# Kernel optimization log

Hardware: AMD Instinct MI355X
Metric: run time of the kernel (lower is better)

Reference implementation:

```python
import jax, jax.numpy as jnp
import numpy as np
import math

B, S, D = 8, 2048, 1024  # batch, seq_len, d_model (num_heads=1 -> d_k=d_v=D)

def _trunc_normal(key, shape, fan_in, fan_out):
    std = math.sqrt(2.0 / (fan_in + fan_out))
    return jax.random.truncated_normal(key, -3.0, 3.0, shape, jnp.float32) * std

def setup_inputs() -> dict:
    key = jax.random.key(0)
    kx, kq, kk, kv, ko = jax.random.split(key, 5)
    return {
        "in_features": jax.random.normal(kx, (B, S, D), jnp.float32),
        "Wq": _trunc_normal(kq, (D, D), D, D),  # Linear stores (out, in)
        "Wk": _trunc_normal(kk, (D, D), D, D),
        "Wv": _trunc_normal(kv, (D, D), D, D),
        "Wo": _trunc_normal(ko, (D, D), D, D),
    }

def reference(in_features, Wq, Wk, Wv, Wo):
    d_k = Wq.shape[0]
    scale = 1.0 / math.sqrt(d_k)
    x = in_features  # [B,S,D]; num_heads=1 so head split/merge are identities
    Q = x @ Wq.T  # [B,S,d_k]
    K = x @ Wk.T
    V = x @ Wv.T
    scores = jnp.einsum('bqd,bkd->bqk', Q, K) * scale  # [B,S,S]
    seq_len = x.shape[-2]
    causal = jnp.tril(jnp.ones((seq_len, seq_len), dtype=bool))
    scores = jnp.where(causal, scores, -jnp.inf)
    attn = jax.nn.softmax(scores, axis=-1)  # stable max-shift softmax, same as run_softmax
    out = jnp.einsum('bqk,bkd->bqd', attn, V)  # [B,S,d_v]
    return out @ Wo.T  # [B,S,D]
```

## Files before the change

kernel.cpp:

```cpp
#include <hip/hip_runtime.h>
#include <hip/hip_bf16.h>
#include <cstdint>


typedef short    bf16x8 __attribute__((ext_vector_type(8)));
typedef _Float16 f16x8  __attribute__((ext_vector_type(8)));
typedef _Float16 f16x4  __attribute__((ext_vector_type(4)));
typedef float    f32x4  __attribute__((ext_vector_type(4)));

#define S_LEN 2048
#define D_DIM 1024
#define M_ROWS 16384
#define NT_Q 16
#define SLOTS 136
#define SLOT_ELEMS 16384
#define PBATCH ((size_t)SLOTS * SLOT_ELEMS)

__device__ __forceinline__ ushort f32_to_bf16_rne(float f) {
    uint32_t u = __float_as_uint(f);
    uint32_t r = (u + 0x7FFFu + ((u >> 16) & 1u)) >> 16;
    return (ushort)r;
}

__device__ __forceinline__ void gload_lds16(const void* g, void* l) {
    __builtin_amdgcn_global_load_lds(
        (const __attribute__((address_space(1))) uint32_t*)(const uint32_t*)g,
        (__attribute__((address_space(3))) uint32_t*)(uint32_t*)l, 16, 0, 0);
}

__global__ void cast_f32_bf16(const float* __restrict__ in,
                              ushort* __restrict__ out, int n4) {
    int i = blockIdx.x * blockDim.x + threadIdx.x;
    if (i < n4) {
        float4 v = ((const float4*)in)[i];
        ushort4 o;
        o.x = f32_to_bf16_rne(v.x);
        o.y = f32_to_bf16_rne(v.y);
        o.z = f32_to_bf16_rne(v.z);
        o.w = f32_to_bf16_rne(v.w);
        ((ushort4*)out)[i] = o;
    }
}

template <int MODE>
__global__ __launch_bounds__(256)
void gemm_bt(const ushort* __restrict__ A, const ushort* __restrict__ B,
             void* __restrict__ C) {
    __shared__ ushort As[128 * 32];
    __shared__ ushort Bs[128 * 32];

    const int t  = threadIdx.x;
    const int tm = blockIdx.x;
    const int tn = blockIdx.y;
    const int l  = t & 63;
    const int w  = t >> 6;
    const int wr = w >> 1, wc = w & 1;
    const int lr = l & 15;
    const int lk = (l >> 4) << 3;

    f32x4 acc[4][4] = {};

    const int arow = t >> 2;
    const int akc  = (t & 3) << 3;
    const ushort* Ag = A + (size_t)(tm * 128 + arow) * D_DIM + akc;
    const ushort* Bg = B + (size_t)(tn * 128 + arow) * D_DIM + akc;
    ushort* Al = &As[arow * 32 + akc];
    ushort* Bl = &Bs[arow * 32 + akc];

    for (int k0 = 0; k0 < D_DIM; k0 += 32) {
        __syncthreads();
        gload_lds16(Ag + k0,              Al);
        gload_lds16(Ag + k0 + 64 * D_DIM, Al + 64 * 32);
        gload_lds16(Bg + k0,              Bl);
        gload_lds16(Bg + k0 + 64 * D_DIM, Bl + 64 * 32);
        __syncthreads();

        bf16x8 af[4], bf[4];
#pragma unroll
        for (int m = 0; m < 4; ++m)
            af[m] = *(const bf16x8*)&As[(wr * 64 + m * 16 + lr) * 32 + lk];
#pragma unroll
        for (int n = 0; n < 4; ++n)
            bf[n] = *(const bf16x8*)&Bs[(wc * 64 + n * 16 + lr) * 32 + lk];
#pragma unroll
        for (int n = 0; n < 4; ++n)
#pragma unroll
            for (int m = 0; m < 4; ++m)
                acc[n][m] = __builtin_amdgcn_mfma_f32_16x16x32_bf16(
                    bf[n], af[m], acc[n][m], 0, 0, 0);
    }

    const int cr = (l >> 4) << 2;
#pragma unroll
    for (int n = 0; n < 4; ++n) {
#pragma unroll
        for (int m = 0; m < 4; ++m) {
            const int row  = tm * 128 + wr * 64 + m * 16 + lr;
            const int col0 = tn * 128 + wc * 64 + n * 16 + cr;
            f32x4 v = acc[n][m];
            if (MODE == 0) {
                ushort4 o;
                o.x = f32_to_bf16_rne(v[0]);
                o.y = f32_to_bf16_rne(v[1]);
                o.z = f32_to_bf16_rne(v[2]);
                o.w = f32_to_bf16_rne(v[3]);
                *(ushort4*)((ushort*)C + (size_t)row * D_DIM + col0) = o;
            } else if (MODE == 2) {
                *(f32x4*)((float*)C + (size_t)row * D_DIM + col0) = v;
            } else {
                const int b = row >> 11;
                const int s = row & 2047;
                _Float16* Vt = (_Float16*)C;
                size_t base = ((size_t)b * D_DIM + col0) * S_LEN + s;
#pragma unroll
                for (int r = 0; r < 4; ++r)
                    Vt[base + (size_t)r * S_LEN] = (_Float16)v[r];
            }
        }
    }
}

__global__ __launch_bounds__(256)
void gemm_qk(const ushort* __restrict__ Q, const ushort* __restrict__ K,
             _Float16* __restrict__ P) {
    __shared__ ushort As[128 * 32];
    __shared__ ushort Bs[128 * 32];

    const int b = blockIdx.y;
    const int s = blockIdx.x;
    int tm = (int)((sqrtf(8.0f * (float)s + 1.0f) - 1.0f) * 0.5f);
    while ((tm + 1) * (tm + 2) / 2 <= s) ++tm;
    while (tm * (tm + 1) / 2 > s) --tm;
    const int tn = s - tm * (tm + 1) / 2;

    const int t  = threadIdx.x;
    const int l  = t & 63;
    const int w  = t >> 6;
    const int wr = w >> 1, wc = w & 1;
    const int lr = l & 15;
    const int lk = (l >> 4) << 3;

    f32x4 acc[4][4] = {};

    const int arow = t >> 2;
    const int akc  = (t & 3) << 3;
    const ushort* Ag = Q + ((size_t)b * S_LEN + tm * 128 + arow) * D_DIM + akc;
    const ushort* Bg = K + ((size_t)b * S_LEN + tn * 128 + arow) * D_DIM + akc;
    ushort* Al = &As[arow * 32 + akc];
    ushort* Bl = &Bs[arow * 32 + akc];

    for (int k0 = 0; k0 < D_DIM; k0 += 32) {
        __syncthreads();
        gload_lds16(Ag + k0,              Al);
        gload_lds16(Ag + k0 + 64 * D_DIM, Al + 64 * 32);
        gload_lds16(Bg + k0,              Bl);
        gload_lds16(Bg + k0 + 64 * D_DIM, Bl + 64 * 32);
        __syncthreads();

        bf16x8 af[4], bf[4];
#pragma unroll
        for (int m = 0; m < 4; ++m)
            af[m] = *(const bf16x8*)&As[(wr * 64 + m * 16 + lr) * 32 + lk];
#pragma unroll
        for (int n = 0; n < 4; ++n)
            bf[n] = *(const bf16x8*)&Bs[(wc * 64 + n * 16 + lr) * 32 + lk];
#pragma unroll
        for (int n = 0; n < 4; ++n)
#pragma unroll
            for (int m = 0; m < 4; ++m)
                acc[n][m] = __builtin_amdgcn_mfma_f32_16x16x32_bf16(
                    bf[n], af[m], acc[n][m], 0, 0, 0);
    }

    _Float16* slot = P + (size_t)b * PBATCH + (size_t)s * SLOT_ELEMS;
    const int cr = (l >> 4) << 2;
    const float scale = 0.03125f;
#pragma unroll
    for (int n = 0; n < 4; ++n) {
#pragma unroll
        for (int m = 0; m < 4; ++m) {
            const int row_l  = wr * 64 + m * 16 + lr;
            const int col0_l = wc * 64 + n * 16 + cr;
            f32x4 v = acc[n][m];
            f16x4 o;
#pragma unroll
            for (int r = 0; r < 4; ++r) {
                float sv = v[r] * scale;
                if (tm == tn && (col0_l + r) > row_l) sv = -30000.0f;
                o[r] = (_Float16)sv;
            }
            *(f16x4*)(slot + (size_t)row_l * 128 + col0_l) = o;
        }
    }
}

__global__ __launch_bounds__(256)
void softmax_rows(_Float16* __restrict__ P) {
    const int b  = blockIdx.y;
    const int q  = blockIdx.x;
    const int tm = q >> 7;
    const int nchunk = (tm + 1) * 16;
    _Float16* row = P + (size_t)b * PBATCH +
                    ((size_t)(tm * (tm + 1) / 2)) * SLOT_ELEMS +
                    (size_t)(q & 127) * 128;

    const int t = threadIdx.x;
    const bool active = t < nchunk;
    _Float16* addr = row + (size_t)(t >> 4) * SLOT_ELEMS + (t & 15) * 8;

    float v[8];
    float mx = -1e30f;
    if (active) {
        f16x8 h = *(const f16x8*)addr;
#pragma unroll
        for (int i = 0; i < 8; ++i) {
            v[i] = (float)h[i];
            mx = fmaxf(mx, v[i]);
        }
    }
#pragma unroll
    for (int d = 1; d < 64; d <<= 1) mx = fmaxf(mx, __shfl_xor(mx, d));
    __shared__ float redm[4], reds[4];
    if ((t & 63) == 0) redm[t >> 6] = mx;
    __syncthreads();
    mx = fmaxf(fmaxf(redm[0], redm[1]), fmaxf(redm[2], redm[3]));

    float sum = 0.0f;
    if (active) {
#pragma unroll
        for (int i = 0; i < 8; ++i) {
            v[i] = __expf(v[i] - mx);
            sum += v[i];
        }
    }
#pragma unroll
    for (int d = 1; d < 64; d <<= 1) sum += __shfl_xor(sum, d);
    if ((t & 63) == 0) reds[t >> 6] = sum;
    __syncthreads();
    sum = reds[0] + reds[1] + reds[2] + reds[3];
    const float inv = 1.0f / sum;

    if (active) {
        f16x8 h;
#pragma unroll
        for (int i = 0; i < 8; ++i) h[i] = (_Float16)(v[i] * inv);
        *(f16x8*)addr = h;
    }
}

__global__ __launch_bounds__(256)
void gemm_pv(const _Float16* __restrict__ P, const _Float16* __restrict__ Vt,
             ushort* __restrict__ O) {
    __shared__ _Float16 As[128 * 32];
    __shared__ _Float16 Bs[128 * 32];

    const int b  = blockIdx.y;
    const int tm = NT_Q - 1 - (blockIdx.x >> 3);
    const int dn = blockIdx.x & 7;
    const int KN = (tm + 1) * 128;

    const int t  = threadIdx.x;
    const int l  = t & 63;
    const int w  = t >> 6;
    const int wr = w >> 1, wc = w & 1;
    const int lr = l & 15;
    const int lk = (l >> 4) << 3;

    f32x4 acc[4][4] = {};

    const int arow = t >> 2;
    const int akc  = (t & 3) << 3;
    const _Float16* Prow = P + (size_t)b * PBATCH +
                           ((size_t)(tm * (tm + 1) / 2)) * SLOT_ELEMS;
    const _Float16* Vb = Vt + ((size_t)b * D_DIM + dn * 128 + arow) * S_LEN;
    _Float16* Al = &As[arow * 32 + akc];
    _Float16* Bl = &Bs[arow * 32 + akc];

    for (int k0 = 0; k0 < KN; k0 += 32) {
        const _Float16* Ag = Prow + (size_t)(k0 >> 7) * SLOT_ELEMS +
                             (size_t)arow * 128 + (k0 & 127) + akc;
        __syncthreads();
        gload_lds16(Ag,            Al);
        gload_lds16(Ag + 64 * 128, Al + 64 * 32);
        gload_lds16(Vb + k0 + akc,               Bl);
        gload_lds16(Vb + k0 + akc + 64 * S_LEN,  Bl + 64 * 32);
        __syncthreads();

        f16x8 af[4], bf[4];
#pragma unroll
        for (int m = 0; m < 4; ++m)
            af[m] = *(const f16x8*)&As[(wr * 64 + m * 16 + lr) * 32 + lk];
#pragma unroll
        for (int n = 0; n < 4; ++n)
            bf[n] = *(const f16x8*)&Bs[(wc * 64 + n * 16 + lr) * 32 + lk];
#pragma unroll
        for (int n = 0; n < 4; ++n)
#pragma unroll
            for (int m = 0; m < 4; ++m)
                acc[n][m] = __builtin_amdgcn_mfma_f32_16x16x32_f16(
                    bf[n], af[m], acc[n][m], 0, 0, 0);
    }

    const int cr = (l >> 4) << 2;
#pragma unroll
    for (int n = 0; n < 4; ++n) {
#pragma unroll
        for (int m = 0; m < 4; ++m) {
            const int row  = tm * 128 + wr * 64 + m * 16 + lr;
            const int col0 = dn * 128 + wc * 64 + n * 16 + cr;
            f32x4 v = acc[n][m];
            ushort4 o;
            o.x = f32_to_bf16_rne(v[0]);
            o.y = f32_to_bf16_rne(v[1]);
            o.z = f32_to_bf16_rne(v[2]);
            o.w = f32_to_bf16_rne(v[3]);
            *(ushort4*)(O + ((size_t)b * S_LEN + row) * D_DIM + col0) = o;
        }
    }
}

extern "C" void kernel_launch(void* const* d_in, const int* in_sizes, int n_in,
                              void* d_out, int out_size, void* d_ws,
                              size_t ws_size, hipStream_t stream) {
    const float* x  = (const float*)d_in[0];
    const float* Wq = (const float*)d_in[1];
    const float* Wk = (const float*)d_in[2];
    const float* Wv = (const float*)d_in[3];
    const float* Wo = (const float*)d_in[4];

    char* ws = (char*)d_ws;
    size_t off = 0;
    ushort*    xb  = (ushort*)(ws + off);    off += (size_t)M_ROWS * D_DIM * 2;
    ushort*    Wqb = (ushort*)(ws + off);    off += (size_t)D_DIM * D_DIM * 2;
    ushort*    Wkb = (ushort*)(ws + off);    off += (size_t)D_DIM * D_DIM * 2;
    ushort*    Wvb = (ushort*)(ws + off);    off += (size_t)D_DIM * D_DIM * 2;
    ushort*    Wob = (ushort*)(ws + off);    off += (size_t)D_DIM * D_DIM * 2;
    ushort*    Qb  = (ushort*)(ws + off);    off += (size_t)M_ROWS * D_DIM * 2;
    ushort*    Kb  = (ushort*)(ws + off);    off += (size_t)M_ROWS * D_DIM * 2;
    _Float16*  Vtb = (_Float16*)(ws + off);  off += (size_t)M_ROWS * D_DIM * 2;
    _Float16*  Pb  = (_Float16*)(ws + off);  off += (size_t)8 * PBATCH * 2;

    cast_f32_bf16<<<(M_ROWS * D_DIM / 4 + 255) / 256, 256, 0, stream>>>(
        x, xb, M_ROWS * D_DIM / 4);
    cast_f32_bf16<<<(D_DIM * D_DIM / 4 + 255) / 256, 256, 0, stream>>>(
        Wq, Wqb, D_DIM * D_DIM / 4);
    cast_f32_bf16<<<(D_DIM * D_DIM / 4 + 255) / 256, 256, 0, stream>>>(
        Wk, Wkb, D_DIM * D_DIM / 4);
    cast_f32_bf16<<<(D_DIM * D_DIM / 4 + 255) / 256, 256, 0, stream>>>(
        Wv, Wvb, D_DIM * D_DIM / 4);
    cast_f32_bf16<<<(D_DIM * D_DIM / 4 + 255) / 256, 256, 0, stream>>>(
        Wo, Wob, D_DIM * D_DIM / 4);

    dim3 gg(M_ROWS / 128, D_DIM / 128);
    gemm_bt<0><<<gg, 256, 0, stream>>>(xb, Wqb, Qb);
    gemm_bt<0><<<gg, 256, 0, stream>>>(xb, Wkb, Kb);
    gemm_bt<1><<<gg, 256, 0, stream>>>(xb, Wvb, Vtb);

    gemm_qk<<<dim3(SLOTS, 8), 256, 0, stream>>>(Qb, Kb, Pb);
    softmax_rows<<<dim3(S_LEN, 8), 256, 0, stream>>>(Pb);
    gemm_pv<<<dim3(128, 8), 256, 0, stream>>>(Pb, Vtb, xb);

    gemm_bt<2><<<gg, 256, 0, stream>>>(xb, Wob, (float*)d_out);
}
```

Measured before the change: 532.1 us.

## Fuse QKV projections, widen PV tiles, swizzle block order, batch weight casts

The three QKV projection GEMMs become one 512-thread kernel that loads each x tile once and multiplies it against all three weight tiles, cutting x reads by a factor of three. The PV GEMM now computes a 128x256 output tile per block, halving P reloads at the cost of more accumulator registers. Block indices in the projection, QK and output GEMMs are remapped so neighbouring blocks land on different XCDs for better cache locality. The four weight casts are merged into one launch. The larger register footprint in the fused kernels may lower occupancy.

```diff
diff --git a/kernel.cpp b/kernel.cpp
--- a/kernel.cpp
+++ b/kernel.cpp
@@ -42,75 +42,117 @@
     }
 }
 
-template <int MODE>
-__global__ __launch_bounds__(256)
-void gemm_bt(const ushort* __restrict__ A, const ushort* __restrict__ B,
-             void* __restrict__ C) {
+__global__ void cast4_f32_bf16(const float* __restrict__ w0,
+                               const float* __restrict__ w1,
+                               const float* __restrict__ w2,
+                               const float* __restrict__ w3,
+                               ushort* __restrict__ o0, ushort* __restrict__ o1,
+                               ushort* __restrict__ o2, ushort* __restrict__ o3,
+                               int n4) {
+    const int s = blockIdx.y;
+    const float* in  = (s == 0) ? w0 : (s == 1) ? w1 : (s == 2) ? w2 : w3;
+    ushort*      out = (s == 0) ? o0 : (s == 1) ? o1 : (s == 2) ? o2 : o3;
+    int i = blockIdx.x * blockDim.x + threadIdx.x;
+    if (i < n4) {
+        float4 v = ((const float4*)in)[i];
+        ushort4 o;
+        o.x = f32_to_bf16_rne(v.x);
+        o.y = f32_to_bf16_rne(v.y);
+        o.z = f32_to_bf16_rne(v.z);
+        o.w = f32_to_bf16_rne(v.w);
+        ((ushort4*)out)[i] = o;
+    }
+}
+
+__global__ __launch_bounds__(512)
+void gemm_qkv3(const ushort* __restrict__ A, const ushort* __restrict__ Wq,
+               const ushort* __restrict__ Wk, const ushort* __restrict__ Wv,
+               ushort* __restrict__ Qo, ushort* __restrict__ Ko,
+               _Float16* __restrict__ Vt) {
     __shared__ ushort As[128 * 32];
-    __shared__ ushort Bs[128 * 32];
+    __shared__ ushort Bs[3][128 * 32];
+
+    const int bid = blockIdx.x;
+    const int g   = (bid & 7) * 128 + (bid >> 3);
+    const int tm  = g >> 3;
+    const int tn  = g & 7;
 
     const int t  = threadIdx.x;
-    const int tm = blockIdx.x;
-    const int tn = blockIdx.y;
     const int l  = t & 63;
     const int w  = t >> 6;
-    const int wr = w >> 1, wc = w & 1;
+    const int wr = w >> 2;
+    const int wc = w & 3;
     const int lr = l & 15;
     const int lk = (l >> 4) << 3;
 
-    f32x4 acc[4][4] = {};
+    f32x4 acc[3][4][2] = {};
 
     const int arow = t >> 2;
-    const int akc  = (t & 3) << 3;
-    const ushort* Ag = A + (size_t)(tm * 128 + arow) * D_DIM + akc;
-    const ushort* Bg = B + (size_t)(tn * 128 + arow) * D_DIM + akc;
-    ushort* Al = &As[arow * 32 + akc];
-    ushort* Bl = &Bs[arow * 32 + akc];
+    const int acol = (t & 3) << 3;
+    const ushort* Ag  = A  + (size_t)(tm * 128 + arow) * D_DIM + acol;
+    const ushort* Bg0 = Wq + (size_t)(tn * 128 + arow) * D_DIM + acol;
+    const ushort* Bg1 = Wk + (size_t)(tn * 128 + arow) * D_DIM + acol;
+    const ushort* Bg2 = Wv + (size_t)(tn * 128 + arow) * D_DIM + acol;
+    ushort* Al  = &As[t * 8];
+    ushort* Bl0 = &Bs[0][t * 8];
+    ushort* Bl1 = &Bs[1][t * 8];
+    ushort* Bl2 = &Bs[2][t * 8];
 
     for (int k0 = 0; k0 < D_DIM; k0 += 32) {
         __syncthreads();
-        gload_lds16(Ag + k0,              Al);
-        gload_lds16(Ag + k0 + 64 * D_DIM, Al + 64 * 32);
-        gload_lds16(Bg + k0,              Bl);
-        gload_lds16(Bg + k0 + 64 * D_DIM, Bl + 64 * 32);
-        __syncthreads();
-
-        bf16x8 af[4], bf[4];
+        gload_lds16(Ag + k0,  Al);
+        gload_lds16(Bg0 + k0, Bl0);
+        gload_lds16(Bg1 + k0, Bl1);
+        gload_lds16(Bg2 + k0, Bl2);
+        __syncthreads();
+
+        bf16x8 af[4];
 #pragma unroll
         for (int m = 0; m < 4; ++m)
             af[m] = *(const bf16x8*)&As[(wr * 64 + m * 16 + lr) * 32 + lk];
 #pragma unroll
-        for (int n = 0; n < 4; ++n)
-            bf[n] = *(const bf16x8*)&Bs[(wc * 64 + n * 16 + lr) * 32 + lk];
-#pragma unroll
-        for (int n = 0; n < 4; ++n)
-#pragma unroll
-            for (int m = 0; m < 4; ++m)
-                acc[n][m] = __builtin_amdgcn_mfma_f32_16x16x32_bf16(
-                    bf[n], af[m], acc[n][m], 0, 0, 0);
+        for (int w3 = 0; w3 < 3; ++w3) {
+            bf16x8 b0 = *(const bf16x8*)&Bs[w3][(wc * 32 + lr) * 32 + lk];
+            bf16x8 b1 = *(const bf16x8*)&Bs[w3][(wc * 32 + 16 + lr) * 32 + lk];
+#pragma unroll
+            for (int m = 0; m < 4; ++m) {
+                acc[w3][m][0] = __builtin_amdgcn_mfma_f32_16x16x32_bf16(
+                    b0, af[m], acc[w3][m][0], 0, 0, 0);
+                acc[w3][m][1] = __builtin_amdgcn_mfma_f32_16x16x32_bf16(
+                    b1, af[m], acc[w3][m][1], 0, 0, 0);
+            }
+        }
     }
 
     const int cr = (l >> 4) << 2;
 #pragma unroll
-    for (int n = 0; n < 4; ++n) {
-#pragma unroll
-        for (int m = 0; m < 4; ++m) {
+    for (int m = 0; m < 4; ++m) {
+#pragma unroll
+        for (int n = 0; n < 2; ++n) {
             const int row  = tm * 128 + wr * 64 + m * 16 + lr;
-            const int col0 = tn * 128 + wc * 64 + n * 16 + cr;
-            f32x4 v = acc[n][m];
-            if (MODE == 0) {
+            const int col0 = tn * 128 + wc * 32 + n * 16 + cr;
+            {
+                f32x4 v = acc[0][m][n];
                 ushort4 o;
                 o.x = f32_to_bf16_rne(v[0]);
                 o.y = f32_to_bf16_rne(v[1]);
                 o.z = f32_to_bf16_rne(v[2]);
                 o.w = f32_to_bf16_rne(v[3]);
-                *(ushort4*)((ushort*)C + (size_t)row * D_DIM + col0) = o;
-            } else if (MODE == 2) {
-                *(f32x4*)((float*)C + (size_t)row * D_DIM + col0) = v;
-            } else {
+                *(ushort4*)(Qo + (size_t)row * D_DIM + col0) = o;
+            }
+            {
+                f32x4 v = acc[1][m][n];
+                ushort4 o;
+                o.x = f32_to_bf16_rne(v[0]);
+                o.y = f32_to_bf16_rne(v[1]);
+                o.z = f32_to_bf16_rne(v[2]);
+                o.w = f32_to_bf16_rne(v[3]);
+                *(ushort4*)(Ko + (size_t)row * D_DIM + col0) = o;
+            }
+            {
+                f32x4 v = acc[2][m][n];
                 const int b = row >> 11;
                 const int s = row & 2047;
-                _Float16* Vt = (_Float16*)C;
                 size_t base = ((size_t)b * D_DIM + col0) * S_LEN + s;
 #pragma unroll
                 for (int r = 0; r < 4; ++r)
@@ -127,7 +169,8 @@
     __shared__ ushort Bs[128 * 32];
 
     const int b = blockIdx.y;
-    const int s = blockIdx.x;
+    const int x = blockIdx.x;
+    const int s = (x & 7) * 17 + (x >> 3);
     int tm = (int)((sqrtf(8.0f * (float)s + 1.0f) - 1.0f) * 0.5f);
     while ((tm + 1) * (tm + 2) / 2 <= s) ++tm;
     while (tm * (tm + 1) / 2 > s) --tm;
@@ -249,15 +292,17 @@
 }
 
 __global__ __launch_bounds__(256)
-void gemm_pv(const _Float16* __restrict__ P, const _Float16* __restrict__ Vt,
-             ushort* __restrict__ O) {
+void gemm_pv2(const _Float16* __restrict__ P, const _Float16* __restrict__ Vt,
+              ushort* __restrict__ O) {
     __shared__ _Float16 As[128 * 32];
-    __shared__ _Float16 Bs[128 * 32];
-
-    const int b  = blockIdx.y;
-    const int tm = NT_Q - 1 - (blockIdx.x >> 3);
-    const int dn = blockIdx.x & 7;
-    const int KN = (tm + 1) * 128;
+    __shared__ _Float16 Bs[256 * 32];
+
+    const int b   = blockIdx.y;
+    const int x   = blockIdx.x;
+    const int g   = (x & 7) * 8 + (x >> 3);
+    const int tm  = NT_Q - 1 - (g >> 2);
+    const int dn2 = g & 3;
+    const int KN  = (tm + 1) * 128;
 
     const int t  = threadIdx.x;
     const int l  = t & 63;
@@ -266,49 +311,50 @@
     const int lr = l & 15;
     const int lk = (l >> 4) << 3;
 
-    f32x4 acc[4][4] = {};
+    f32x4 acc[4][8] = {};
 
     const int arow = t >> 2;
-    const int akc  = (t & 3) << 3;
+    const int acol = (t & 3) << 3;
     const _Float16* Prow = P + (size_t)b * PBATCH +
                            ((size_t)(tm * (tm + 1) / 2)) * SLOT_ELEMS;
-    const _Float16* Vb = Vt + ((size_t)b * D_DIM + dn * 128 + arow) * S_LEN;
-    _Float16* Al = &As[arow * 32 + akc];
-    _Float16* Bl = &Bs[arow * 32 + akc];
+    const _Float16* Vb = Vt + ((size_t)b * D_DIM + dn2 * 256 + arow) * S_LEN;
+    _Float16* Al = &As[t * 8];
+    _Float16* Bl = &Bs[t * 8];
 
     for (int k0 = 0; k0 < KN; k0 += 32) {
         const _Float16* Ag = Prow + (size_t)(k0 >> 7) * SLOT_ELEMS +
-                             (size_t)arow * 128 + (k0 & 127) + akc;
+                             (size_t)arow * 128 + (k0 & 127) + acol;
         __syncthreads();
         gload_lds16(Ag,            Al);
         gload_lds16(Ag + 64 * 128, Al + 64 * 32);
-        gload_lds16(Vb + k0 + akc,               Bl);
-        gload_lds16(Vb + k0 + akc + 64 * S_LEN,  Bl + 64 * 32);
-        __syncthreads();
-
-        f16x8 af[4], bf[4];
+        gload_lds16(Vb + k0 + acol,                 Bl);
+        gload_lds16(Vb + k0 + acol + 64 * S_LEN,    Bl + 64 * 32);
+        gload_lds16(Vb + k0 + acol + 128 * S_LEN,   Bl + 128 * 32);
+        gload_lds16(Vb + k0 + acol + 192 * S_LEN,   Bl + 192 * 32);
+        __syncthreads();
+
+        f16x8 af[4];
 #pragma unroll
         for (int m = 0; m < 4; ++m)
             af[m] = *(const f16x8*)&As[(wr * 64 + m * 16 + lr) * 32 + lk];
 #pragma unroll
-        for (int n = 0; n < 4; ++n)
-            bf[n] = *(const f16x8*)&Bs[(wc * 64 + n * 16 + lr) * 32 + lk];
-#pragma unroll
-        for (int n = 0; n < 4; ++n)
+        for (int n = 0; n < 8; ++n) {
+            f16x8 bv = *(const f16x8*)&Bs[(wc * 128 + n * 16 + lr) * 32 + lk];
 #pragma unroll
             for (int m = 0; m < 4; ++m)
-                acc[n][m] = __builtin_amdgcn_mfma_f32_16x16x32_f16(
-                    bf[n], af[m], acc[n][m], 0, 0, 0);
+                acc[m][n] = __builtin_amdgcn_mfma_f32_16x16x32_f16(
+                    bv, af[m], acc[m][n], 0, 0, 0);
+        }
     }
 
     const int cr = (l >> 4) << 2;
 #pragma unroll
-    for (int n = 0; n < 4; ++n) {
-#pragma unroll
-        for (int m = 0; m < 4; ++m) {
+    for (int m = 0; m < 4; ++m) {
+#pragma unroll
+        for (int n = 0; n < 8; ++n) {
             const int row  = tm * 128 + wr * 64 + m * 16 + lr;
-            const int col0 = dn * 128 + wc * 64 + n * 16 + cr;
-            f32x4 v = acc[n][m];
+            const int col0 = dn2 * 256 + wc * 128 + n * 16 + cr;
+            f32x4 v = acc[m][n];
             ushort4 o;
             o.x = f32_to_bf16_rne(v[0]);
             o.y = f32_to_bf16_rne(v[1]);
@@ -317,6 +363,67 @@
             *(ushort4*)(O + ((size_t)b * S_LEN + row) * D_DIM + col0) = o;
         }
     }
+}
+
+__global__ __launch_bounds__(256)
+void gemm_out(const ushort* __restrict__ A, const ushort* __restrict__ B,
+              float* __restrict__ C) {
+    __shared__ ushort As[128 * 32];
+    __shared__ ushort Bs[128 * 32];
+
+    const int bid = blockIdx.x;
+    const int g   = (bid & 7) * 128 + (bid >> 3);
+    const int tm  = g >> 3;
+    const int tn  = g & 7;
+
+    const int t  = threadIdx.x;
+    const int l  = t & 63;
+    const int w  = t >> 6;
+    const int wr = w >> 1, wc = w & 1;
+    const int lr = l & 15;
+    const int lk = (l >> 4) << 3;
+
+    f32x4 acc[4][4] = {};
+
+    const int arow = t >> 2;
+    const int akc  = (t & 3) << 3;
+    const ushort* Ag = A + (size_t)(tm * 128 + arow) * D_DIM + akc;
+    const ushort* Bg = B + (size_t)(tn * 128 + arow) * D_DIM + akc;
+    ushort* Al = &As[arow * 32 + akc];
+    ushort* Bl = &Bs[arow * 32 + akc];
+
+    for (int k0 = 0; k0 < D_DIM; k0 += 32) {
+        __syncthreads();
+        gload_lds16(Ag + k0,              Al);
+        gload_lds16(Ag + k0 + 64 * D_DIM, Al + 64 * 32);
+        gload_lds16(Bg + k0,              Bl);
+        gload_lds16(Bg + k0 + 64 * D_DIM, Bl + 64 * 32);
+        __syncthreads();
+
+        bf16x8 af[4], bf[4];
+#pragma unroll
+        for (int m = 0; m < 4; ++m)
+            af[m] = *(const bf16x8*)&As[(wr * 64 + m * 16 + lr) * 32 + lk];
+#pragma unroll
+        for (int n = 0; n < 4; ++n)
+            bf[n] = *(const bf16x8*)&Bs[(wc * 64 + n * 16 + lr) * 32 + lk];
+#pragma unroll
+        for (int n = 0; n < 4; ++n)
+#pragma unroll
+            for (int m = 0; m < 4; ++m)
+                acc[n][m] = __builtin_amdgcn_mfma_f32_16x16x32_bf16(
+                    bf[n], af[m], acc[n][m], 0, 0, 0);
+    }
+
+    const int cr = (l >> 4) << 2;
+#pragma unroll
+    for (int n = 0; n < 4; ++n)
+#pragma unroll
+        for (int m = 0; m < 4; ++m) {
+            const int row  = tm * 128 + wr * 64 + m * 16 + lr;
+            const int col0 = tn * 128 + wc * 64 + n * 16 + cr;
+            *(f32x4*)(C + (size_t)row * D_DIM + col0) = acc[n][m];
+        }
 }
 
 extern "C" void kernel_launch(void* const* d_in, const int* in_sizes, int n_in,
@@ -342,23 +449,14 @@
 
     cast_f32_bf16<<<(M_ROWS * D_DIM / 4 + 255) / 256, 256, 0, stream>>>(
         x, xb, M_ROWS * D_DIM / 4);
-    cast_f32_bf16<<<(D_DIM * D_DIM / 4 + 255) / 256, 256, 0, stream>>>(
-        Wq, Wqb, D_DIM * D_DIM / 4);
-    cast_f32_bf16<<<(D_DIM * D_DIM / 4 + 255) / 256, 256, 0, stream>>>(
-        Wk, Wkb, D_DIM * D_DIM / 4);
-    cast_f32_bf16<<<(D_DIM * D_DIM / 4 + 255) / 256, 256, 0, stream>>>(
-        Wv, Wvb, D_DIM * D_DIM / 4);
-    cast_f32_bf16<<<(D_DIM * D_DIM / 4 + 255) / 256, 256, 0, stream>>>(
-        Wo, Wob, D_DIM * D_DIM / 4);
-
-    dim3 gg(M_ROWS / 128, D_DIM / 128);
-    gemm_bt<0><<<gg, 256, 0, stream>>>(xb, Wqb, Qb);
-    gemm_bt<0><<<gg, 256, 0, stream>>>(xb, Wkb, Kb);
-    gemm_bt<1><<<gg, 256, 0, stream>>>(xb, Wvb, Vtb);
+    cast4_f32_bf16<<<dim3((D_DIM * D_DIM / 4 + 255) / 256, 4), 256, 0, stream>>>(
+        Wq, Wk, Wv, Wo, Wqb, Wkb, Wvb, Wob, D_DIM * D_DIM / 4);
+
+    gemm_qkv3<<<1024, 512, 0, stream>>>(xb, Wqb, Wkb, Wvb, Qb, Kb, Vtb);
 
     gemm_qk<<<dim3(SLOTS, 8), 256, 0, stream>>>(Qb, Kb, Pb);
     softmax_rows<<<dim3(S_LEN, 8), 256, 0, stream>>>(Pb);
-    gemm_pv<<<dim3(128, 8), 256, 0, stream>>>(Pb, Vtb, xb);
-
-    gemm_bt<2><<<gg, 256, 0, stream>>>(xb, Wob, (float*)d_out);
-}
+    gemm_pv2<<<dim3(64, 8), 256, 0, stream>>>(Pb, Vtb, xb);
+
+    gemm_out<<<1024, 256, 0, stream>>>(xb, Wob, (float*)d_out);
+}
```

Result: slower. 556.9 us (+4.7%).
